# Optimization experiments

Hardware: AMD Instinct MI355X
Metric: run time of the kernel (lower is better)

The kernel has to match this reference:

```python
import jax, jax.numpy as jnp
import numpy as np

TAO = 24
M = 7


def setup_inputs() -> dict:
    key = jax.random.key(0)
    k1, k2, k3 = jax.random.split(key, 3)
    B, S, C = 32, 2048, 7
    d_model = 512
    cm = C * (M + 1)  # 56 conv input channels
    x = jax.random.normal(k1, (B, S, C), dtype=jnp.float32)
    # total_conv: Conv1d(in=cm, out=d_model, kernel=3), kaiming_normal fan_in, leaky_relu
    fan_in = cm * 3
    gain = float(np.sqrt(2.0 / (1.0 + 0.01 ** 2)))
    std = gain / float(np.sqrt(fan_in))
    W = jax.random.normal(k2, (d_model, cm, 3), dtype=jnp.float32) * std
    bound = 1.0 / float(np.sqrt(fan_in))
    b = jax.random.uniform(k3, (d_model,), dtype=jnp.float32, minval=-bound, maxval=bound)
    return {"x": x, "W": W, "b": b}


def reference(x, W, b):
    B, S, C = x.shape
    mt = M * TAO  # delay-embedding lookback = 168
    n_valid = S - mt
    # sliding delay-embedding gather: for t in [mt, S), take x[t - k*tao] for k=0..M
    t_idx = jnp.arange(mt, S)                       # [n_valid]
    offs = jnp.arange(M + 1) * TAO                  # [M+1]
    tidx = t_idx[:, None] - offs[None, :]           # [n_valid, M+1]
    ext = x[:, tidx, :]                             # [B, n_valid, M+1, C]
    # torch reshape order: (n_valid, C, M+1) -> C major, offset minor
    fv = jnp.transpose(ext, (0, 1, 3, 2)).reshape(B, n_valid, C * (M + 1))
    # left-pad time axis with zeros to restore seq_len
    fv = jnp.pad(fv, ((0, 0), (mt, 0), (0, 0)))     # [B, S, C*(M+1)]
    # circular Conv1d (kernel 3, pad 1 circular)
    z = jnp.transpose(fv, (0, 2, 1))                # [B, C*(M+1), S]
    zp = jnp.pad(z, ((0, 0), (0, 0), (1, 1)), mode="wrap")
    out = jax.lax.conv_general_dilated(
        zp, W, window_strides=(1,), padding="VALID",
        dimension_numbers=("NCH", "OIH", "NCH"))    # [B, d_model, S]
    out = out + b[None, :, None]
    return jnp.transpose(out, (0, 2, 1))            # [B, S, d_model]
```

## Files before the change

### kernel.cpp

```cpp
#include <hip/hip_runtime.h>
#include <hip/hip_bf16.h>
#include <stdint.h>


#define TAO    24
#define MTAPS  7
#define C_IN   7
#define SEQ    2048
#define DMODEL 512
#define KP     72
#define RB     144
#define NROWS  65536
#define BO     128
#define BT     128
#define AROWS  130
#define A_CHUNKS (AROWS * 9)

typedef __attribute__((ext_vector_type(8))) short frag_ab;
typedef __attribute__((ext_vector_type(4))) float frag_cd;

__global__ __launch_bounds__(256)
void prep_kernel(const float* __restrict__ x, const float* __restrict__ W,
                 __hip_bfloat16* __restrict__ G, __hip_bfloat16* __restrict__ Wf)
{
    const int tid = threadIdx.x;
    if (blockIdx.x < 256) {
        const int row = blockIdx.x * 256 + tid;
        const int b   = row >> 11;
        const int t   = row & (SEQ - 1);
        const float* xb = x + b * (SEQ * C_IN);

        union { __hip_bfloat16 h[KP]; int4 v[9]; } u;
#pragma unroll
        for (int j = 0; j < 9; j++) u.v[j] = (int4){0, 0, 0, 0};

        if (t >= MTAPS * TAO) {
#pragma unroll
            for (int m = 0; m < 8; m++) {
                const float* p = xb + (t - TAO * m) * C_IN;
#pragma unroll
                for (int c = 0; c < C_IN; c++)
                    u.h[c * 8 + m] = __float2bfloat16(p[c]);
            }
        }
        int4* dst = (int4*)((char*)G + (size_t)row * RB);
#pragma unroll
        for (int j = 0; j < 9; j++) dst[j] = u.v[j];
    } else {
        const int idx  = (blockIdx.x - 256) * 256 + tid;
        const int lane = idx & 63;
        const int kc   = (idx >> 6) & 1;
        const int oc   = (idx >> 7) & 31;
        const int h    = idx >> 12;
        const int o    = oc * 16 + (lane & 15);
        const int kof  = kc * 32 + (lane >> 4) * 8;

        union { __hip_bfloat16 s[8]; int4 v; } u;
#pragma unroll
        for (int j = 0; j < 8; j++) {
            const int k = kof + j;
            float v = (k < 56) ? W[o * 168 + k * 3 + h] : 0.0f;
            u.s[j] = __float2bfloat16(v);
        }
        ((int4*)Wf)[idx] = u.v;
    }
}

__global__ __launch_bounds__(256, 3)
void gemm_kernel(const __hip_bfloat16* __restrict__ G,
                 const __hip_bfloat16* __restrict__ Wf,
                 const float* __restrict__ bias,
                 float* __restrict__ out)
{
    __shared__ __align__(16) char As[AROWS * RB];

    const int tid = threadIdx.x;
    const int bo  = blockIdx.x & 3;
    const int mb  = blockIdx.x >> 2;
    const int b   = mb >> 4;
    const int t0  = (mb & 15) * BT;
    const int o0  = bo * BO;

    {
        const char* Gb = (const char*)G + (size_t)b * SEQ * RB;
        for (int q = tid; q < A_CHUNKS; q += 256) {
            const int row = q / 9;
            const int c16 = q - row * 9;
            const int srow = (t0 - 1 + row + SEQ) & (SEQ - 1);
            __builtin_amdgcn_global_load_lds(
                (const __attribute__((address_space(1))) uint32_t*)(Gb + (size_t)srow * RB + c16 * 16),
                (__attribute__((address_space(3))) uint32_t*)(As + q * 16), 16, 0, 0);
        }
    }

    const int wave = tid >> 6;
    const int lane = tid & 63;
    const int wo   = (wave >> 1) * 64;
    const int wt   = (wave & 1) * 64;
    const int l15  = lane & 15;
    const int quad = lane >> 4;

    float4 bias4[4];
#pragma unroll
    for (int mi = 0; mi < 4; mi++)
        bias4[mi] = *(const float4*)&bias[o0 + wo + mi * 16 + quad * 4];

    frag_cd acc[4][4];
#pragma unroll
    for (int i = 0; i < 4; i++)
#pragma unroll
        for (int j = 0; j < 4; j++)
            acc[i][j] = (frag_cd){0.f, 0.f, 0.f, 0.f};

    __syncthreads();

    const int octile = bo * 8 + (wo >> 4);
#pragma unroll
    for (int h = 0; h < 3; h++) {
#pragma unroll
        for (int kc = 0; kc < 2; kc++) {
            frag_ab wfr[4], gfr[4];
#pragma unroll
            for (int mi = 0; mi < 4; mi++) {
                const int tile = (h * 32 + octile + mi) * 2 + kc;
                wfr[mi] = *(const frag_ab*)((const char*)Wf + (size_t)tile * 1024 + lane * 16);
            }
            const int kbyte = kc * 64 + quad * 16;
#pragma unroll
            for (int ni = 0; ni < 4; ni++)
                gfr[ni] = *(const frag_ab*)(As + (wt + ni * 16 + l15 + h) * RB + kbyte);
#pragma unroll
            for (int mi = 0; mi < 4; mi++)
#pragma unroll
                for (int ni = 0; ni < 4; ni++)
                    acc[mi][ni] = __builtin_amdgcn_mfma_f32_16x16x32_bf16(
                        wfr[mi], gfr[ni], acc[mi][ni], 0, 0, 0);
        }
    }

    const size_t rowbase = (size_t)b * SEQ + t0 + wt;
#pragma unroll
    for (int ni = 0; ni < 4; ni++) {
        const size_t r = rowbase + ni * 16 + l15;
        float* orow = out + r * DMODEL + o0 + wo + quad * 4;
#pragma unroll
        for (int mi = 0; mi < 4; mi++) {
            float4 v;
            v.x = acc[mi][ni][0] + bias4[mi].x;
            v.y = acc[mi][ni][1] + bias4[mi].y;
            v.z = acc[mi][ni][2] + bias4[mi].z;
            v.w = acc[mi][ni][3] + bias4[mi].w;
            *(float4*)(orow + mi * 16) = v;
        }
    }
}

#define KDIM  168
#define KPAD  192
#define FLDK  200
__global__ __launch_bounds__(256, 1)
void fused_tokenconv_kernel(const float* __restrict__ x,
                            const float* __restrict__ W,
                            const float* __restrict__ bias,
                            float* __restrict__ out)
{
    __shared__ __hip_bfloat16 As[128][FLDK];
    __shared__ __hip_bfloat16 Bs[128][FLDK];
    const int tid = threadIdx.x;
    const int blk = blockIdx.x;
    const int nb  = blk & 3;
    const int mb  = blk >> 2;
    const int b   = mb >> 4;
    const int t0  = (mb & 15) * 128;
    const int o0  = nb * 128;
    const float* xb = x + b * (SEQ * C_IN);

    for (int idx = tid; idx < 128 * KPAD; idx += 256) {
        int o_l = idx / KPAD;
        int i   = idx - o_l * KPAD;
        float v = (i < KDIM) ? W[(o0 + o_l) * KDIM + i] : 0.0f;
        Bs[o_l][i] = __float2bfloat16(v);
    }
    for (int idx = tid; idx < 128 * KPAD; idx += 256) {
        int t_l = idx / KPAD;
        int i   = idx - t_l * KPAD;
        float v = 0.0f;
        if (i < KDIM) {
            int c = i / 24;
            int r = i - c * 24;
            int m = r / 3;
            int h = r - m * 3;
            int s = (t0 + t_l + h - 1 + SEQ) & (SEQ - 1);
            if (s >= MTAPS * TAO) v = xb[(s - TAO * m) * C_IN + c];
        }
        As[t_l][i] = __float2bfloat16(v);
    }
    __syncthreads();

    const int wave = tid >> 6;
    const int lane = tid & 63;
    const int wm   = (wave >> 1) * 64;
    const int wn   = (wave & 1) * 64;
    const int l15  = lane & 15;
    const int quad = lane >> 4;

    frag_cd acc[4][4];
#pragma unroll
    for (int i = 0; i < 4; i++)
#pragma unroll
        for (int j = 0; j < 4; j++)
            acc[i][j] = (frag_cd){0.f, 0.f, 0.f, 0.f};

#pragma unroll
    for (int kc = 0; kc < KPAD / 32; kc++) {
        const int kof = kc * 32 + quad * 8;
        frag_ab a[4], bf[4];
#pragma unroll
        for (int mi = 0; mi < 4; mi++)
            a[mi] = *(const frag_ab*)&As[wm + mi * 16 + l15][kof];
#pragma unroll
        for (int ni = 0; ni < 4; ni++)
            bf[ni] = *(const frag_ab*)&Bs[wn + ni * 16 + l15][kof];
#pragma unroll
        for (int mi = 0; mi < 4; mi++)
#pragma unroll
            for (int ni = 0; ni < 4; ni++)
                acc[mi][ni] = __builtin_amdgcn_mfma_f32_16x16x32_bf16(
                    a[mi], bf[ni], acc[mi][ni], 0, 0, 0);
    }
    float* outb = out + (size_t)b * SEQ * DMODEL;
#pragma unroll
    for (int ni = 0; ni < 4; ni++) {
        const int o  = o0 + wn + ni * 16 + l15;
        const float bvv = bias[o];
#pragma unroll
        for (int mi = 0; mi < 4; mi++) {
#pragma unroll
            for (int reg = 0; reg < 4; reg++) {
                const int t = t0 + wm + mi * 16 + quad * 4 + reg;
                outb[(size_t)t * DMODEL + o] = acc[mi][ni][reg] + bvv;
            }
        }
    }
}

extern "C" void kernel_launch(void* const* d_in, const int* in_sizes, int n_in,
                              void* d_out, int out_size, void* d_ws, size_t ws_size,
                              hipStream_t stream) {
    const float* x    = (const float*)d_in[0];
    const float* W    = (const float*)d_in[1];
    const float* bias = (const float*)d_in[2];
    float* out        = (float*)d_out;

    const size_t g_bytes = (size_t)NROWS * RB;
    const size_t w_bytes = (size_t)12288 * 16;
    if (ws_size >= g_bytes + w_bytes) {
        __hip_bfloat16* G  = (__hip_bfloat16*)d_ws;
        __hip_bfloat16* Wf = (__hip_bfloat16*)((char*)d_ws + g_bytes);
        hipLaunchKernelGGL(prep_kernel, dim3(304), dim3(256), 0, stream, x, W, G, Wf);
        hipLaunchKernelGGL(gemm_kernel, dim3((DMODEL / BO) * (NROWS / BT)), dim3(256), 0, stream,
                           G, Wf, bias, out);
    } else {
        hipLaunchKernelGGL(fused_tokenconv_kernel, dim3(32 * 16 * 4), dim3(256), 0, stream,
                           x, W, bias, out);
    }
}
```

Before: 158.4 us.

## Build delay-embedding fragments in-kernel from raw x instead of a materialized G buffer

Removes the intermediate G matrix (65536 rows × 144 bytes of bf16 delay embeddings) and its prep pass. The GEMM kernel now loads a 298-row window of raw x into shared memory as channel-major bf16 planes. Each B fragment is then gathered with strided LDS reads at offsets of 24 taps, with masking for the zero-padded lookback region. This cuts global write and read traffic and one kernel's work. In exchange, each fragment now takes eight scalar 2-byte LDS reads instead of one 16-byte vector load, and the windows are reloaded redundantly by the four output-column blocks.

New measurement: 153.5 us. 1.03x faster.

```diff
diff --git a/kernel.cpp b/kernel.cpp
--- a/kernel.cpp
+++ b/kernel.cpp
@@ -8,71 +8,43 @@
 #define C_IN   7
 #define SEQ    2048
 #define DMODEL 512
-#define KP     72
-#define RB     144
 #define NROWS  65536
 #define BO     128
 #define BT     128
-#define AROWS  130
-#define A_CHUNKS (AROWS * 9)
+#define XROWS  298
+#define XPLANE 304
 
 typedef __attribute__((ext_vector_type(8))) short frag_ab;
 typedef __attribute__((ext_vector_type(4))) float frag_cd;
 
 __global__ __launch_bounds__(256)
-void prep_kernel(const float* __restrict__ x, const float* __restrict__ W,
-                 __hip_bfloat16* __restrict__ G, __hip_bfloat16* __restrict__ Wf)
+void prep_w_kernel(const float* __restrict__ W, __hip_bfloat16* __restrict__ Wf)
 {
-    const int tid = threadIdx.x;
-    if (blockIdx.x < 256) {
-        const int row = blockIdx.x * 256 + tid;
-        const int b   = row >> 11;
-        const int t   = row & (SEQ - 1);
-        const float* xb = x + b * (SEQ * C_IN);
-
-        union { __hip_bfloat16 h[KP]; int4 v[9]; } u;
-#pragma unroll
-        for (int j = 0; j < 9; j++) u.v[j] = (int4){0, 0, 0, 0};
-
-        if (t >= MTAPS * TAO) {
-#pragma unroll
-            for (int m = 0; m < 8; m++) {
-                const float* p = xb + (t - TAO * m) * C_IN;
-#pragma unroll
-                for (int c = 0; c < C_IN; c++)
-                    u.h[c * 8 + m] = __float2bfloat16(p[c]);
-            }
-        }
-        int4* dst = (int4*)((char*)G + (size_t)row * RB);
-#pragma unroll
-        for (int j = 0; j < 9; j++) dst[j] = u.v[j];
-    } else {
-        const int idx  = (blockIdx.x - 256) * 256 + tid;
-        const int lane = idx & 63;
-        const int kc   = (idx >> 6) & 1;
-        const int oc   = (idx >> 7) & 31;
-        const int h    = idx >> 12;
-        const int o    = oc * 16 + (lane & 15);
-        const int kof  = kc * 32 + (lane >> 4) * 8;
-
-        union { __hip_bfloat16 s[8]; int4 v; } u;
-#pragma unroll
-        for (int j = 0; j < 8; j++) {
-            const int k = kof + j;
-            float v = (k < 56) ? W[o * 168 + k * 3 + h] : 0.0f;
-            u.s[j] = __float2bfloat16(v);
-        }
-        ((int4*)Wf)[idx] = u.v;
-    }
+    const int idx  = blockIdx.x * 256 + threadIdx.x;
+    const int lane = idx & 63;
+    const int kc   = (idx >> 6) & 1;
+    const int oc   = (idx >> 7) & 31;
+    const int h    = idx >> 12;
+    const int o    = oc * 16 + (lane & 15);
+    const int kof  = kc * 32 + (lane >> 4) * 8;
+
+    union { __hip_bfloat16 s[8]; int4 v; } u;
+#pragma unroll
+    for (int j = 0; j < 8; j++) {
+        const int k = kof + j;
+        float v = (k < 56) ? W[o * 168 + k * 3 + h] : 0.0f;
+        u.s[j] = __float2bfloat16(v);
+    }
+    ((int4*)Wf)[idx] = u.v;
 }
 
 __global__ __launch_bounds__(256, 3)
-void gemm_kernel(const __hip_bfloat16* __restrict__ G,
+void gemm_kernel(const float* __restrict__ x,
                  const __hip_bfloat16* __restrict__ Wf,
                  const float* __restrict__ bias,
                  float* __restrict__ out)
 {
-    __shared__ __align__(16) char As[AROWS * RB];
+    __shared__ short xt[8 * XPLANE];
 
     const int tid = threadIdx.x;
     const int bo  = blockIdx.x & 3;
@@ -82,14 +54,19 @@
     const int o0  = bo * BO;
 
     {
-        const char* Gb = (const char*)G + (size_t)b * SEQ * RB;
-        for (int q = tid; q < A_CHUNKS; q += 256) {
-            const int row = q / 9;
-            const int c16 = q - row * 9;
-            const int srow = (t0 - 1 + row + SEQ) & (SEQ - 1);
-            __builtin_amdgcn_global_load_lds(
-                (const __attribute__((address_space(1))) uint32_t*)(Gb + (size_t)srow * RB + c16 * 16),
-                (__attribute__((address_space(3))) uint32_t*)(As + q * 16), 16, 0, 0);
+        const float* xb = x + b * (SEQ * C_IN);
+        const int base = (t0 - 169 + SEQ) & (SEQ - 1);
+#pragma unroll
+        for (int it = 0; it < 9; it++) {
+            const int idx = it * 256 + tid;
+            if (idx < XROWS * C_IN) {
+                const int r = idx / 7;
+                const int c = idx - r * 7;
+                const int xrow = (base + r) & (SEQ - 1);
+                const float v = xb[xrow * C_IN + c];
+                __hip_bfloat16 bv = __float2bfloat16(v);
+                xt[c * XPLANE + r] = *reinterpret_cast<short*>(&bv);
+            }
         }
     }
 
@@ -119,22 +96,34 @@
     for (int h = 0; h < 3; h++) {
 #pragma unroll
         for (int kc = 0; kc < 2; kc++) {
-            frag_ab wfr[4], gfr[4];
+            const int qp = kc * 4 + quad;
+            frag_ab wfr[4];
 #pragma unroll
             for (int mi = 0; mi < 4; mi++) {
                 const int tile = (h * 32 + octile + mi) * 2 + kc;
                 wfr[mi] = *(const frag_ab*)((const char*)Wf + (size_t)tile * 1024 + lane * 16);
             }
-            const int kbyte = kc * 64 + quad * 16;
-#pragma unroll
-            for (int ni = 0; ni < 4; ni++)
-                gfr[ni] = *(const frag_ab*)(As + (wt + ni * 16 + l15 + h) * RB + kbyte);
+            union { short s[8]; frag_ab f; int4 i4; } g[4];
+#pragma unroll
+            for (int ni = 0; ni < 4; ni++) {
+                const int lbase = wt + ni * 16 + l15 + h;
+                const int ttw = (t0 + lbase - 1 + SEQ) & (SEQ - 1);
+                const short* p = &xt[qp * XPLANE + lbase];
+#pragma unroll
+                for (int j = 0; j < 8; j++)
+                    g[ni].s[j] = p[168 - 24 * j];
+                const bool valid = (ttw >= MTAPS * TAO) && (qp < 7);
+                g[ni].i4.x = valid ? g[ni].i4.x : 0;
+                g[ni].i4.y = valid ? g[ni].i4.y : 0;
+                g[ni].i4.z = valid ? g[ni].i4.z : 0;
+                g[ni].i4.w = valid ? g[ni].i4.w : 0;
+            }
 #pragma unroll
             for (int mi = 0; mi < 4; mi++)
 #pragma unroll
                 for (int ni = 0; ni < 4; ni++)
                     acc[mi][ni] = __builtin_amdgcn_mfma_f32_16x16x32_bf16(
-                        wfr[mi], gfr[ni], acc[mi][ni], 0, 0, 0);
+                        wfr[mi], g[ni].f, acc[mi][ni], 0, 0, 0);
         }
     }
 
@@ -252,14 +241,12 @@
     const float* bias = (const float*)d_in[2];
     float* out        = (float*)d_out;
 
-    const size_t g_bytes = (size_t)NROWS * RB;
     const size_t w_bytes = (size_t)12288 * 16;
-    if (ws_size >= g_bytes + w_bytes) {
-        __hip_bfloat16* G  = (__hip_bfloat16*)d_ws;
-        __hip_bfloat16* Wf = (__hip_bfloat16*)((char*)d_ws + g_bytes);
-        hipLaunchKernelGGL(prep_kernel, dim3(304), dim3(256), 0, stream, x, W, G, Wf);
+    if (ws_size >= w_bytes) {
+        __hip_bfloat16* Wf = (__hip_bfloat16*)d_ws;
+        hipLaunchKernelGGL(prep_w_kernel, dim3(48), dim3(256), 0, stream, W, Wf);
         hipLaunchKernelGGL(gemm_kernel, dim3((DMODEL / BO) * (NROWS / BT)), dim3(256), 0, stream,
-                           G, Wf, bias, out);
+                           x, Wf, bias, out);
     } else {
         hipLaunchKernelGGL(fused_tokenconv_kernel, dim3(32 * 16 * 4), dim3(256), 0, stream,
                            x, W, bias, out);
```
